# Performance work log

Hardware: AMD Instinct MI355X
Metric: run time of the kernel (lower is better)

The kernel has to match this reference:

```python
import jax, jax.numpy as jnp
import numpy as np

B, S, E, H = 2, 2048, 1024, 16
DH = E // H
SCALE = 1.0 / float(np.sqrt(E))  # note: original scales by 1/sqrt(hidden_dim), not head_dim


def _icl_mask(s):
    # triu(diagonal=0) is masked (-inf): only strictly-past positions visible,
    # except (0,0) which is explicitly unmasked so row 0 attends to itself.
    m = jnp.triu(jnp.ones((s, s), dtype=bool), k=0)
    return m.at[0, 0].set(False)


def setup_inputs() -> dict:
    key = jax.random.key(0)
    ks = jax.random.split(key, 7)
    mk = lambda k, shp: jax.random.normal(k, shp, dtype=jnp.float32)
    return {
        "q": mk(ks[0], (B, S, E)),
        "k": mk(ks[1], (B, S, E)),
        "v": mk(ks[2], (B, S, E)),
        "Wq": mk(ks[3], (E, E)) * 0.02,
        "Wk": mk(ks[4], (E, E)) * 0.02,
        "Wv": mk(ks[5], (E, E)) * 0.02,
        "Wo": mk(ks[6], (E, E)) * 0.02,
    }


def reference(q, k, v, Wq, Wk, Wv, Wo):
    b, s, e = q.shape
    h, dh = H, e // H
    # projections (nn.Linear: x @ W.T), split heads -> [b, h, s, dh]
    qh = (q @ Wq.T).reshape(b, s, h, dh).transpose(0, 2, 1, 3)
    kh = (k @ Wk.T).reshape(b, s, h, dh).transpose(0, 2, 1, 3)
    vh = (v @ Wv.T).reshape(b, s, h, dh).transpose(0, 2, 1, 3)
    scores = jnp.einsum("bhsd,bhtd->bhst", qh, kh) * SCALE  # [b,h,s,s]
    scores = jnp.where(_icl_mask(s), -jnp.inf, scores)
    probs = jax.nn.softmax(scores, axis=-1)
    out = jnp.einsum("bhst,bhtd->bhsd", probs, vh)
    out = out.transpose(0, 2, 1, 3).reshape(b, s, e)
    return out @ Wo.T
```

## Files before the change

kernel.cpp:

```cpp
#include <hip/hip_runtime.h>
#include <hip/hip_bf16.h>

typedef unsigned short u16;
typedef unsigned int u32;
typedef __bf16 bf16x8 __attribute__((ext_vector_type(8)));
typedef float float4_ __attribute__((ext_vector_type(4)));

#define B_ 2
#define S_ 2048
#define E_ 1024
#define H_ 16
#define DH_ 64
#define M_ (B_*S_)
#define SCALE_ 0.03125f
#define LOG2E_ 1.4426950408889634f

__device__ __forceinline__ u16 f2bf(float f) {
    unsigned int x = __float_as_uint(f);
    x += 0x7fffu + ((x >> 16) & 1u);
    return (u16)(x >> 16);
}

template <typename T> struct raw8;
template <> struct raw8<float> { float4_ lo, hi; };
template <> struct raw8<u16>   { bf16x8 v; };

__device__ __forceinline__ raw8<float> ldr8(const float* p) {
    raw8<float> r; const float4_* q = (const float4_*)p; r.lo = q[0]; r.hi = q[1]; return r;
}
__device__ __forceinline__ raw8<u16> ldr8(const u16* p) {
    raw8<u16> r; r.v = *(const bf16x8*)p; return r;
}
__device__ __forceinline__ bf16x8 cvt8(const raw8<u16>& r) { return r.v; }
__device__ __forceinline__ bf16x8 cvt8(const raw8<float>& r) {
    union { bf16x8 v; __hip_bfloat162 h[4]; } u;
    u.h[0] = __float22bfloat162_rn(float2{r.lo[0], r.lo[1]});
    u.h[1] = __float22bfloat162_rn(float2{r.lo[2], r.lo[3]});
    u.h[2] = __float22bfloat162_rn(float2{r.hi[0], r.hi[1]});
    u.h[3] = __float22bfloat162_rn(float2{r.hi[2], r.hi[3]});
    return u.v;
}
__device__ __forceinline__ bf16x8 ld8(const u16* p) { return *(const bf16x8*)p; }

__device__ __forceinline__ void async16(u16* lds, const u16* g) {
    __builtin_amdgcn_global_load_lds(
        (const __attribute__((address_space(1))) u32*)g,
        (__attribute__((address_space(3))) u32*)lds, 16, 0, 0);
}

__device__ __forceinline__ int swz32(int row, int col) {
    return row * 32 + ((((col >> 3) ^ (row & 3)) << 3) | (col & 7));
}

__global__ __launch_bounds__(256)
void convw_kernel(const float* __restrict__ Wq, const float* __restrict__ Wk,
                  const float* __restrict__ Wv, const float* __restrict__ Wo,
                  u16* __restrict__ Wqb, u16* __restrict__ Wkb,
                  u16* __restrict__ Wvb, u16* __restrict__ Wob) {
    const int which = blockIdx.y;
    const float* src = which == 0 ? Wq : which == 1 ? Wk : which == 2 ? Wv : Wo;
    u16* dst        = which == 0 ? Wqb : which == 1 ? Wkb : which == 2 ? Wvb : Wob;
    size_t off = ((size_t)blockIdx.x * 256 + threadIdx.x) * 8;
    *(bf16x8*)&dst[off] = cvt8(ldr8(&src[off]));
}

__global__ __launch_bounds__(256)
void proj_kernel(const float* __restrict__ q, const float* __restrict__ k, const float* __restrict__ v,
                 const u16* __restrict__ Wqb, const u16* __restrict__ Wkb, const u16* __restrict__ Wvb,
                 u16* __restrict__ Qh, u16* __restrict__ Kh, u16* __restrict__ Vt) {
    const int z = blockIdx.z;
    const float* A = (z == 0) ? q : (z == 1) ? k : v;
    const u16* Wb  = (z == 0) ? Wqb : (z == 1) ? Wkb : Wvb;
    u16* C         = (z == 0) ? Qh : (z == 1) ? Kh : Vt;
    const float cscale = (z == 0) ? SCALE_ : 1.0f;
    const int transV = (z == 2);
    const int bm = blockIdx.x * 128, bn = blockIdx.y * 128;

    __shared__ u16 As[2][128 * 32];
    __shared__ u16 Bs[2][128 * 32];

    const int tid  = threadIdx.x;
    const int lane = tid & 63;
    const int w    = tid >> 6;
    const int wr   = (w >> 1) * 64, wc = (w & 1) * 64;
    const int m16  = lane & 15, quad = lane >> 4, q4 = quad * 4;
    const int row0 = tid >> 2, kc0 = (tid & 3) * 8, row1 = row0 + 64;
    const int c1   = tid + 256;
    const int r1   = c1 >> 2;

    const u16* wg0 = &Wb[(size_t)(bn + row0) * 1024 + (size_t)(((tid & 3) ^ (row0 & 3)) * 8)];
    const u16* wg1 = &Wb[(size_t)(bn + r1)   * 1024 + (size_t)(((c1 & 3) ^ (r1 & 3)) * 8)];

    float4_ acc[4][4];
#pragma unroll
    for (int i = 0; i < 4; i++)
#pragma unroll
        for (int j = 0; j < 4; j++) acc[i][j] = (float4_){0.f, 0.f, 0.f, 0.f};

    raw8<float> pa0 = ldr8(&A[(size_t)(bm + row0) * 1024 + kc0]);
    raw8<float> pa1 = ldr8(&A[(size_t)(bm + row1) * 1024 + kc0]);

    async16((u16*)((char*)Bs[0] + (size_t)tid * 16), wg0);
    async16((u16*)((char*)Bs[0] + (size_t)c1 * 16), wg1);
    *(bf16x8*)&As[0][swz32(row0, kc0)] = cvt8(pa0);
    *(bf16x8*)&As[0][swz32(row1, kc0)] = cvt8(pa1);
    pa0 = ldr8(&A[(size_t)(bm + row0) * 1024 + 32 + kc0]);
    pa1 = ldr8(&A[(size_t)(bm + row1) * 1024 + 32 + kc0]);
    __syncthreads();

    auto step = [&](int t, const u16* Asc, const u16* Bsc, u16* Asn, u16* Bsn) {
        if (t < 31) {
            async16((u16*)((char*)Bsn + (size_t)tid * 16), wg0 + (t + 1) * 32);
            async16((u16*)((char*)Bsn + (size_t)c1 * 16), wg1 + (t + 1) * 32);
            *(bf16x8*)&Asn[swz32(row0, kc0)] = cvt8(pa0);
            *(bf16x8*)&Asn[swz32(row1, kc0)] = cvt8(pa1);
            if (t < 30) {
                pa0 = ldr8(&A[(size_t)(bm + row0) * 1024 + (t + 2) * 32 + kc0]);
                pa1 = ldr8(&A[(size_t)(bm + row1) * 1024 + (t + 2) * 32 + kc0]);
            }
        }
        __builtin_amdgcn_sched_barrier(0);
        bf16x8 af[4], bfr[4];
#pragma unroll
        for (int rt = 0; rt < 4; rt++)
            af[rt] = *(const bf16x8*)&Asc[swz32(wr + rt * 16 + m16, quad * 8)];
#pragma unroll
        for (int ct = 0; ct < 4; ct++)
            bfr[ct] = *(const bf16x8*)&Bsc[swz32(wc + ct * 16 + m16, quad * 8)];
#pragma unroll
        for (int rt = 0; rt < 4; rt++)
#pragma unroll
            for (int ct = 0; ct < 4; ct++)
                acc[rt][ct] = __builtin_amdgcn_mfma_f32_16x16x32_bf16(af[rt], bfr[ct], acc[rt][ct], 0, 0, 0);
        if (t < 31) __syncthreads();
    };

    for (int t = 0; t < 32; t += 2) {
        step(t,     As[0], Bs[0], As[1], Bs[1]);
        step(t + 1, As[1], Bs[1], As[0], Bs[0]);
    }

#pragma unroll
    for (int rt = 0; rt < 4; rt++)
#pragma unroll
        for (int ct = 0; ct < 4; ct++)
#pragma unroll
            for (int r = 0; r < 4; r++) {
                int row = bm + wr + rt * 16 + q4 + r;
                int col = bn + wc + ct * 16 + m16;
                u16 val = f2bf(acc[rt][ct][r] * cscale);
                if (!transV) {
                    C[(size_t)row * 1024 + col] = val;
                } else {
                    int bb = row >> 11, s = row & 2047;
                    C[((size_t)(bb * 1024 + col)) * 2048 + s] = val;
                }
            }
}

__global__ __launch_bounds__(256)
void out_kernel(const u16* __restrict__ AO, const u16* __restrict__ Wob, float* __restrict__ C) {
    const int bm = blockIdx.x * 128, bn = blockIdx.y * 64;

    __shared__ u16 As[2][128 * 32];
    __shared__ u16 Bs[2][64 * 32];

    const int tid  = threadIdx.x;
    const int lane = tid & 63;
    const int w    = tid >> 6;
    const int m16  = lane & 15, quad = lane >> 4, q4 = quad * 4;
    const int c1   = tid + 256;

    const int swc = (((tid & 3) ^ ((tid >> 2) & 3)) * 8);
    const u16* ag0 = &AO[(size_t)(bm + (tid >> 2)) * 1024 + swc];
    const u16* ag1 = &AO[(size_t)(bm + (c1 >> 2)) * 1024 + swc];
    const u16* bg  = &Wob[(size_t)(bn + (tid >> 2)) * 1024 + swc];

    float4_ acc[2][4];
#pragma unroll
    for (int i = 0; i < 2; i++)
#pragma unroll
        for (int j = 0; j < 4; j++) acc[i][j] = (float4_){0.f, 0.f, 0.f, 0.f};

    async16((u16*)((char*)As[0] + (size_t)tid * 16), ag0);
    async16((u16*)((char*)As[0] + (size_t)c1 * 16), ag1);
    async16((u16*)((char*)Bs[0] + (size_t)tid * 16), bg);
    __syncthreads();

    auto step = [&](int t, const u16* Asc, const u16* Bsc, u16* Asn, u16* Bsn) {
        if (t < 31) {
            async16((u16*)((char*)Asn + (size_t)tid * 16), ag0 + (t + 1) * 32);
            async16((u16*)((char*)Asn + (size_t)c1 * 16), ag1 + (t + 1) * 32);
            async16((u16*)((char*)Bsn + (size_t)tid * 16), bg + (t + 1) * 32);
        }
        __builtin_amdgcn_sched_barrier(0);
        bf16x8 af[2], bfr[4];
#pragma unroll
        for (int rt = 0; rt < 2; rt++)
            af[rt] = *(const bf16x8*)&Asc[swz32(w * 32 + rt * 16 + m16, quad * 8)];
#pragma unroll
        for (int ct = 0; ct < 4; ct++)
            bfr[ct] = *(const bf16x8*)&Bsc[swz32(ct * 16 + m16, quad * 8)];
#pragma unroll
        for (int rt = 0; rt < 2; rt++)
#pragma unroll
            for (int ct = 0; ct < 4; ct++)
                acc[rt][ct] = __builtin_amdgcn_mfma_f32_16x16x32_bf16(af[rt], bfr[ct], acc[rt][ct], 0, 0, 0);
        if (t < 31) __syncthreads();
    };

    for (int t = 0; t < 32; t += 2) {
        step(t,     As[0], Bs[0], As[1], Bs[1]);
        step(t + 1, As[1], Bs[1], As[0], Bs[0]);
    }

#pragma unroll
    for (int rt = 0; rt < 2; rt++)
#pragma unroll
        for (int ct = 0; ct < 4; ct++)
#pragma unroll
            for (int r = 0; r < 4; r++) {
                int row = bm + w * 32 + rt * 16 + q4 + r;
                int col = bn + ct * 16 + m16;
                C[(size_t)row * 1024 + col] = acc[rt][ct][r];
            }
}

__device__ __forceinline__ int sw64(int row, int col) {
    return row * 64 + ((((col >> 3) ^ (row & 7)) << 3) | (col & 7));
}

__global__ __launch_bounds__(256)
void attn_kernel(const u16* __restrict__ Qh, const u16* __restrict__ Kh,
                 const u16* __restrict__ Vt, u16* __restrict__ O) {
    const int h    = blockIdx.x;
    const int pair = blockIdx.y;
    const int tqA  = pair;
    const int tqB  = 31 - pair;
    const int b    = blockIdx.z;
    const int tid  = threadIdx.x;
    const int lane = tid & 63;
    const int w    = tid >> 6;
    const int m16  = lane & 15;
    const int quad = lane >> 4;
    const int q4   = quad * 4;

    __shared__ u16 Ks[2][64 * 64];
    __shared__ u16 Vs[2][64 * 64];
    __shared__ u16 PsA[64 * 64];
    __shared__ u16 PsB[64 * 64];

    const int srow0 = tid >> 3;
    const int skc0  = (tid & 7) * 8;
    const int sblk0 = ((skc0 >> 3) ^ (srow0 & 7)) << 3;
    const int srow1 = srow0 + 32;
    const int sblk1 = ((skc0 >> 3) ^ (srow1 & 7)) << 3;

    const size_t kbase = ((size_t)(b * S_)) * E_ + h * DH_;
    const size_t vbase = ((size_t)(b * 1024 + h * DH_)) * 2048;

    bf16x8 qfA[2], qfB[2];
    {
        const u16* qa = Qh + ((size_t)(b * S_ + tqA * 64 + w * 16 + m16)) * E_ + h * DH_;
        const u16* qb = Qh + ((size_t)(b * S_ + tqB * 64 + w * 16 + m16)) * E_ + h * DH_;
        qfA[0] = ld8(qa + quad * 8);  qfA[1] = ld8(qa + 32 + quad * 8);
        qfB[0] = ld8(qb + quad * 8);  qfB[1] = ld8(qb + 32 + quad * 8);
    }

    float lA[4] = {0.f, 0.f, 0.f, 0.f}, lB[4] = {0.f, 0.f, 0.f, 0.f};
    float4_ oA[4], oB[4];
#pragma unroll
    for (int dt = 0; dt < 4; dt++) { oA[dt] = (float4_){0.f,0.f,0.f,0.f}; oB[dt] = (float4_){0.f,0.f,0.f,0.f}; }

    *(bf16x8*)&Ks[0][srow0 * 64 + sblk0] = ld8(&Kh[kbase + (size_t)srow0 * E_ + skc0]);
    *(bf16x8*)&Ks[0][srow1 * 64 + sblk1] = ld8(&Kh[kbase + (size_t)srow1 * E_ + skc0]);
    *(bf16x8*)&Vs[0][srow0 * 64 + sblk0] = ld8(&Vt[vbase + (size_t)srow0 * 2048 + skc0]);
    *(bf16x8*)&Vs[0][srow1 * 64 + sblk1] = ld8(&Vt[vbase + (size_t)srow1 * 2048 + skc0]);
    __syncthreads();

    for (int t = 0; t <= tqB; t++) {
        const int cur = t & 1;

        bf16x8 kr0, kr1, vr0, vr1;
        const bool havepf = (t < tqB);
        if (havepf) {
            const size_t ko = kbase + (size_t)((t + 1) * 64) * E_;
            kr0 = ld8(&Kh[ko + (size_t)srow0 * E_ + skc0]);
            kr1 = ld8(&Kh[ko + (size_t)srow1 * E_ + skc0]);
            vr0 = ld8(&Vt[vbase + (size_t)srow0 * 2048 + (t + 1) * 64 + skc0]);
            vr1 = ld8(&Vt[vbase + (size_t)srow1 * 2048 + (t + 1) * 64 + skc0]);
        }

        auto process = [&](const bf16x8* qf, float* l_part, float4_* o_acc,
                           u16* Ps, int tqX) {
            const u16* Kc = &Ks[cur][0];
            const u16* Vc = &Vs[cur][0];
            float4_ sc[4];
#pragma unroll
            for (int ct = 0; ct < 4; ct++) sc[ct] = (float4_){0.f,0.f,0.f,0.f};
#pragma unroll
            for (int ks = 0; ks < 2; ks++)
#pragma unroll
                for (int ct = 0; ct < 4; ct++) {
                    bf16x8 kf = *(const bf16x8*)&Kc[sw64(ct * 16 + m16, ks * 32 + quad * 8)];
                    sc[ct] = __builtin_amdgcn_mfma_f32_16x16x32_bf16(qf[ks], kf, sc[ct], 0, 0, 0);
                }

            float p[4][4];
            if (t != tqX) {
#pragma unroll
                for (int ct = 0; ct < 4; ct++)
#pragma unroll
                    for (int r = 0; r < 4; r++) {
                        float pp = exp2f(sc[ct][r] * LOG2E_);
                        p[ct][r] = pp;
                        l_part[r] += pp;
                    }
            } else {
#pragma unroll
                for (int ct = 0; ct < 4; ct++)
#pragma unroll
                    for (int r = 0; r < 4; r++) {
                        int i_loc = w * 16 + q4 + r;
                        int j_loc = ct * 16 + m16;
                        bool allow = (j_loc < i_loc) || (tqX == 0 && i_loc == 0 && j_loc == 0);
                        float pp = allow ? exp2f(sc[ct][r] * LOG2E_) : 0.f;
                        p[ct][r] = pp;
                        l_part[r] += pp;
                    }
            }

#pragma unroll
            for (int ct = 0; ct < 4; ct++)
#pragma unroll
                for (int r = 0; r < 4; r++)
                    Ps[sw64(w * 16 + q4 + r, ct * 16 + m16)] = f2bf(p[ct][r]);

#pragma unroll
            for (int ks = 0; ks < 2; ks++) {
                bf16x8 pf = *(const bf16x8*)&Ps[sw64(w * 16 + m16, ks * 32 + quad * 8)];
#pragma unroll
                for (int dt = 0; dt < 4; dt++) {
                    bf16x8 vf = *(const bf16x8*)&Vc[sw64(dt * 16 + m16, ks * 32 + quad * 8)];
                    o_acc[dt] = __builtin_amdgcn_mfma_f32_16x16x32_bf16(pf, vf, o_acc[dt], 0, 0, 0);
                }
            }
        };

        process(qfB, lB, oB, PsB, tqB);
        if (t <= tqA) process(qfA, lA, oA, PsA, tqA);

        if (havepf) {
            const int nxt = cur ^ 1;
            *(bf16x8*)&Ks[nxt][srow0 * 64 + sblk0] = kr0;
            *(bf16x8*)&Ks[nxt][srow1 * 64 + sblk1] = kr1;
            *(bf16x8*)&Vs[nxt][srow0 * 64 + sblk0] = vr0;
            *(bf16x8*)&Vs[nxt][srow1 * 64 + sblk1] = vr1;
        }
        __syncthreads();
    }

    auto wrout = [&](const float4_* o_acc, const float* l_part, int tqX) {
        const size_t obase = ((size_t)(b * S_ + tqX * 64)) * E_ + h * DH_;
#pragma unroll
        for (int r = 0; r < 4; r++) {
            float l = l_part[r];
#pragma unroll
            for (int msk = 1; msk <= 8; msk <<= 1) l += __shfl_xor(l, msk);
            float inv_l = 1.0f / l;
            int row = w * 16 + q4 + r;
#pragma unroll
            for (int dt = 0; dt < 4; dt++) {
                int col = dt * 16 + m16;
                O[obase + (size_t)row * E_ + col] = f2bf(o_acc[dt][r] * inv_l);
            }
        }
    };
    wrout(oA, lA, tqA);
    wrout(oB, lB, tqB);
}

extern "C" void kernel_launch(void* const* d_in, const int* in_sizes, int n_in,
                              void* d_out, int out_size, void* d_ws, size_t ws_size,
                              hipStream_t stream) {
    const float* q  = (const float*)d_in[0];
    const float* k  = (const float*)d_in[1];
    const float* v  = (const float*)d_in[2];
    const float* Wq = (const float*)d_in[3];
    const float* Wk = (const float*)d_in[4];
    const float* Wv = (const float*)d_in[5];
    const float* Wo = (const float*)d_in[6];

    u16* ws  = (u16*)d_ws;
    u16* Qh  = ws;
    u16* Kh  = ws + (size_t)M_ * E_;
    u16* Vt  = ws + 2 * (size_t)M_ * E_;
    u16* AO  = ws + 3 * (size_t)M_ * E_;
    u16* Wqb = AO;
    u16* Wkb = AO + (size_t)E_ * E_;
    u16* Wvb = AO + 2 * (size_t)E_ * E_;
    u16* Wob = ws + 4 * (size_t)M_ * E_;

    dim3 blk(256);
    convw_kernel<<<dim3(512, 4), blk, 0, stream>>>(Wq, Wk, Wv, Wo, Wqb, Wkb, Wvb, Wob);
    proj_kernel<<<dim3(32, 8, 3), blk, 0, stream>>>(q, k, v, Wqb, Wkb, Wvb, Qh, Kh, Vt);
    attn_kernel<<<dim3(16, 16, 2), blk, 0, stream>>>(Qh, Kh, Vt, AO);
    out_kernel<<<dim3(32, 16), blk, 0, stream>>>(AO, Wob, (float*)d_out);
}
```

Baseline: 226.4 us.

## Pre-convert activations to bf16 and split attention query tiles across 512-thread blocks

Adds a separate conversion kernel that turns the q/k/v activations into bf16 so the projection GEMM can load both operands with async global-to-LDS copies instead of loading fp32 into registers and converting in the main loop. Xq and Xk are staged in the output buffer and Xv in spare workspace. The attention kernel now runs 512 threads per block, with each 4-wave half handling one of the paired query tiles at the same time, where before one set of waves processed both tiles in sequence. This costs an extra kernel launch and a full extra read and write pass over the activations. Waves on the shorter tile sit idle during later iterations but still hit the barriers.

```diff
diff --git a/kernel.cpp b/kernel.cpp
--- a/kernel.cpp
+++ b/kernel.cpp
@@ -12,6 +12,7 @@
 #define H_ 16
 #define DH_ 64
 #define M_ (B_*S_)
+#define E2_ (E_*E_)
 #define SCALE_ 0.03125f
 #define LOG2E_ 1.4426950408889634f
 
@@ -65,11 +66,22 @@
 }
 
 __global__ __launch_bounds__(256)
-void proj_kernel(const float* __restrict__ q, const float* __restrict__ k, const float* __restrict__ v,
+void convx_kernel(const float* __restrict__ q, const float* __restrict__ k,
+                  const float* __restrict__ v,
+                  u16* __restrict__ Xq, u16* __restrict__ Xk, u16* __restrict__ Xv) {
+    const int which = blockIdx.y;
+    const float* src = which == 0 ? q : which == 1 ? k : v;
+    u16* dst        = which == 0 ? Xq : which == 1 ? Xk : Xv;
+    size_t off = ((size_t)blockIdx.x * 256 + threadIdx.x) * 8;
+    *(bf16x8*)&dst[off] = cvt8(ldr8(&src[off]));
+}
+
+__global__ __launch_bounds__(256)
+void proj_kernel(const u16* __restrict__ Xq, const u16* __restrict__ Xk, const u16* __restrict__ Xv,
                  const u16* __restrict__ Wqb, const u16* __restrict__ Wkb, const u16* __restrict__ Wvb,
                  u16* __restrict__ Qh, u16* __restrict__ Kh, u16* __restrict__ Vt) {
     const int z = blockIdx.z;
-    const float* A = (z == 0) ? q : (z == 1) ? k : v;
+    const u16* A   = (z == 0) ? Xq : (z == 1) ? Xk : Xv;
     const u16* Wb  = (z == 0) ? Wqb : (z == 1) ? Wkb : Wvb;
     u16* C         = (z == 0) ? Qh : (z == 1) ? Kh : Vt;
     const float cscale = (z == 0) ? SCALE_ : 1.0f;
@@ -84,12 +96,13 @@
     const int w    = tid >> 6;
     const int wr   = (w >> 1) * 64, wc = (w & 1) * 64;
     const int m16  = lane & 15, quad = lane >> 4, q4 = quad * 4;
-    const int row0 = tid >> 2, kc0 = (tid & 3) * 8, row1 = row0 + 64;
-    const int c1   = tid + 256;
-    const int r1   = c1 >> 2;
-
-    const u16* wg0 = &Wb[(size_t)(bn + row0) * 1024 + (size_t)(((tid & 3) ^ (row0 & 3)) * 8)];
-    const u16* wg1 = &Wb[(size_t)(bn + r1)   * 1024 + (size_t)(((c1 & 3) ^ (r1 & 3)) * 8)];
+
+    const int row0 = tid >> 2, ch = tid & 3, row1 = row0 + 64;
+    const int csw  = ((ch ^ (row0 & 3)) * 8);
+    const u16* ag0 = &A[(size_t)(bm + row0) * 1024 + csw];
+    const u16* ag1 = &A[(size_t)(bm + row1) * 1024 + csw];
+    const u16* wg0 = &Wb[(size_t)(bn + row0) * 1024 + csw];
+    const u16* wg1 = &Wb[(size_t)(bn + row1) * 1024 + csw];
 
     float4_ acc[4][4];
 #pragma unroll
@@ -97,27 +110,19 @@
 #pragma unroll
         for (int j = 0; j < 4; j++) acc[i][j] = (float4_){0.f, 0.f, 0.f, 0.f};
 
-    raw8<float> pa0 = ldr8(&A[(size_t)(bm + row0) * 1024 + kc0]);
-    raw8<float> pa1 = ldr8(&A[(size_t)(bm + row1) * 1024 + kc0]);
-
+    async16((u16*)((char*)As[0] + (size_t)tid * 16), ag0);
+    async16((u16*)((char*)As[0] + (size_t)tid * 16 + 4096), ag1);
     async16((u16*)((char*)Bs[0] + (size_t)tid * 16), wg0);
-    async16((u16*)((char*)Bs[0] + (size_t)c1 * 16), wg1);
-    *(bf16x8*)&As[0][swz32(row0, kc0)] = cvt8(pa0);
-    *(bf16x8*)&As[0][swz32(row1, kc0)] = cvt8(pa1);
-    pa0 = ldr8(&A[(size_t)(bm + row0) * 1024 + 32 + kc0]);
-    pa1 = ldr8(&A[(size_t)(bm + row1) * 1024 + 32 + kc0]);
+    async16((u16*)((char*)Bs[0] + (size_t)tid * 16 + 4096), wg1);
     __syncthreads();
 
     auto step = [&](int t, const u16* Asc, const u16* Bsc, u16* Asn, u16* Bsn) {
         if (t < 31) {
-            async16((u16*)((char*)Bsn + (size_t)tid * 16), wg0 + (t + 1) * 32);
-            async16((u16*)((char*)Bsn + (size_t)c1 * 16), wg1 + (t + 1) * 32);
-            *(bf16x8*)&Asn[swz32(row0, kc0)] = cvt8(pa0);
-            *(bf16x8*)&Asn[swz32(row1, kc0)] = cvt8(pa1);
-            if (t < 30) {
-                pa0 = ldr8(&A[(size_t)(bm + row0) * 1024 + (t + 2) * 32 + kc0]);
-                pa1 = ldr8(&A[(size_t)(bm + row1) * 1024 + (t + 2) * 32 + kc0]);
-            }
+            const size_t ko = (size_t)(t + 1) * 32;
+            async16((u16*)((char*)Asn + (size_t)tid * 16), ag0 + ko);
+            async16((u16*)((char*)Asn + (size_t)tid * 16 + 4096), ag1 + ko);
+            async16((u16*)((char*)Bsn + (size_t)tid * 16), wg0 + ko);
+            async16((u16*)((char*)Bsn + (size_t)tid * 16 + 4096), wg1 + ko);
         }
         __builtin_amdgcn_sched_barrier(0);
         bf16x8 af[4], bfr[4];
@@ -230,74 +235,69 @@
     return row * 64 + ((((col >> 3) ^ (row & 7)) << 3) | (col & 7));
 }
 
-__global__ __launch_bounds__(256)
+__global__ __launch_bounds__(512)
 void attn_kernel(const u16* __restrict__ Qh, const u16* __restrict__ Kh,
                  const u16* __restrict__ Vt, u16* __restrict__ O) {
     const int h    = blockIdx.x;
     const int pair = blockIdx.y;
+    const int b    = blockIdx.z;
     const int tqA  = pair;
     const int tqB  = 31 - pair;
-    const int b    = blockIdx.z;
     const int tid  = threadIdx.x;
     const int lane = tid & 63;
     const int w    = tid >> 6;
+    const int half = w >> 2;
+    const int w4   = w & 3;
+    const int myTq = half ? tqB : tqA;
     const int m16  = lane & 15;
     const int quad = lane >> 4;
     const int q4   = quad * 4;
 
     __shared__ u16 Ks[2][64 * 64];
     __shared__ u16 Vs[2][64 * 64];
-    __shared__ u16 PsA[64 * 64];
-    __shared__ u16 PsB[64 * 64];
-
-    const int srow0 = tid >> 3;
-    const int skc0  = (tid & 7) * 8;
-    const int sblk0 = ((skc0 >> 3) ^ (srow0 & 7)) << 3;
-    const int srow1 = srow0 + 32;
-    const int sblk1 = ((skc0 >> 3) ^ (srow1 & 7)) << 3;
+    __shared__ u16 Ps[2][64 * 64];
+
+    const int srow = tid >> 3;
+    const int skc  = (tid & 7) * 8;
+    const int sblk = ((skc >> 3) ^ (srow & 7)) << 3;
 
     const size_t kbase = ((size_t)(b * S_)) * E_ + h * DH_;
     const size_t vbase = ((size_t)(b * 1024 + h * DH_)) * 2048;
 
-    bf16x8 qfA[2], qfB[2];
+    bf16x8 qf[2];
     {
-        const u16* qa = Qh + ((size_t)(b * S_ + tqA * 64 + w * 16 + m16)) * E_ + h * DH_;
-        const u16* qb = Qh + ((size_t)(b * S_ + tqB * 64 + w * 16 + m16)) * E_ + h * DH_;
-        qfA[0] = ld8(qa + quad * 8);  qfA[1] = ld8(qa + 32 + quad * 8);
-        qfB[0] = ld8(qb + quad * 8);  qfB[1] = ld8(qb + 32 + quad * 8);
+        const u16* qa = Qh + ((size_t)(b * S_ + myTq * 64 + w4 * 16 + m16)) * E_ + h * DH_;
+        qf[0] = ld8(qa + quad * 8);
+        qf[1] = ld8(qa + 32 + quad * 8);
     }
 
-    float lA[4] = {0.f, 0.f, 0.f, 0.f}, lB[4] = {0.f, 0.f, 0.f, 0.f};
-    float4_ oA[4], oB[4];
-#pragma unroll
-    for (int dt = 0; dt < 4; dt++) { oA[dt] = (float4_){0.f,0.f,0.f,0.f}; oB[dt] = (float4_){0.f,0.f,0.f,0.f}; }
-
-    *(bf16x8*)&Ks[0][srow0 * 64 + sblk0] = ld8(&Kh[kbase + (size_t)srow0 * E_ + skc0]);
-    *(bf16x8*)&Ks[0][srow1 * 64 + sblk1] = ld8(&Kh[kbase + (size_t)srow1 * E_ + skc0]);
-    *(bf16x8*)&Vs[0][srow0 * 64 + sblk0] = ld8(&Vt[vbase + (size_t)srow0 * 2048 + skc0]);
-    *(bf16x8*)&Vs[0][srow1 * 64 + sblk1] = ld8(&Vt[vbase + (size_t)srow1 * 2048 + skc0]);
+    float l_part[4] = {0.f, 0.f, 0.f, 0.f};
+    float4_ o_acc[4];
+#pragma unroll
+    for (int dt = 0; dt < 4; dt++) o_acc[dt] = (float4_){0.f, 0.f, 0.f, 0.f};
+
+    *(bf16x8*)&Ks[0][srow * 64 + sblk] = ld8(&Kh[kbase + (size_t)srow * E_ + skc]);
+    *(bf16x8*)&Vs[0][srow * 64 + sblk] = ld8(&Vt[vbase + (size_t)srow * 2048 + skc]);
     __syncthreads();
 
     for (int t = 0; t <= tqB; t++) {
         const int cur = t & 1;
 
-        bf16x8 kr0, kr1, vr0, vr1;
+        bf16x8 kr, vr;
         const bool havepf = (t < tqB);
         if (havepf) {
-            const size_t ko = kbase + (size_t)((t + 1) * 64) * E_;
-            kr0 = ld8(&Kh[ko + (size_t)srow0 * E_ + skc0]);
-            kr1 = ld8(&Kh[ko + (size_t)srow1 * E_ + skc0]);
-            vr0 = ld8(&Vt[vbase + (size_t)srow0 * 2048 + (t + 1) * 64 + skc0]);
-            vr1 = ld8(&Vt[vbase + (size_t)srow1 * 2048 + (t + 1) * 64 + skc0]);
-        }
-
-        auto process = [&](const bf16x8* qf, float* l_part, float4_* o_acc,
-                           u16* Ps, int tqX) {
+            kr = ld8(&Kh[kbase + (size_t)((t + 1) * 64 + srow) * E_ + skc]);
+            vr = ld8(&Vt[vbase + (size_t)srow * 2048 + (t + 1) * 64 + skc]);
+        }
+
+        if (t <= myTq) {
             const u16* Kc = &Ks[cur][0];
             const u16* Vc = &Vs[cur][0];
+            u16* Pm = &Ps[half][0];
+
             float4_ sc[4];
 #pragma unroll
-            for (int ct = 0; ct < 4; ct++) sc[ct] = (float4_){0.f,0.f,0.f,0.f};
+            for (int ct = 0; ct < 4; ct++) sc[ct] = (float4_){0.f, 0.f, 0.f, 0.f};
 #pragma unroll
             for (int ks = 0; ks < 2; ks++)
 #pragma unroll
@@ -307,7 +307,7 @@
                 }
 
             float p[4][4];
-            if (t != tqX) {
+            if (t != myTq) {
 #pragma unroll
                 for (int ct = 0; ct < 4; ct++)
 #pragma unroll
@@ -321,9 +321,9 @@
                 for (int ct = 0; ct < 4; ct++)
 #pragma unroll
                     for (int r = 0; r < 4; r++) {
-                        int i_loc = w * 16 + q4 + r;
+                        int i_loc = w4 * 16 + q4 + r;
                         int j_loc = ct * 16 + m16;
-                        bool allow = (j_loc < i_loc) || (tqX == 0 && i_loc == 0 && j_loc == 0);
+                        bool allow = (j_loc < i_loc) || (myTq == 0 && i_loc == 0 && j_loc == 0);
                         float pp = allow ? exp2f(sc[ct][r] * LOG2E_) : 0.f;
                         p[ct][r] = pp;
                         l_part[r] += pp;
@@ -334,50 +334,41 @@
             for (int ct = 0; ct < 4; ct++)
 #pragma unroll
                 for (int r = 0; r < 4; r++)
-                    Ps[sw64(w * 16 + q4 + r, ct * 16 + m16)] = f2bf(p[ct][r]);
+                    Pm[sw64(w4 * 16 + q4 + r, ct * 16 + m16)] = f2bf(p[ct][r]);
 
 #pragma unroll
             for (int ks = 0; ks < 2; ks++) {
-                bf16x8 pf = *(const bf16x8*)&Ps[sw64(w * 16 + m16, ks * 32 + quad * 8)];
+                bf16x8 pf = *(const bf16x8*)&Pm[sw64(w4 * 16 + m16, ks * 32 + quad * 8)];
 #pragma unroll
                 for (int dt = 0; dt < 4; dt++) {
                     bf16x8 vf = *(const bf16x8*)&Vc[sw64(dt * 16 + m16, ks * 32 + quad * 8)];
                     o_acc[dt] = __builtin_amdgcn_mfma_f32_16x16x32_bf16(pf, vf, o_acc[dt], 0, 0, 0);
                 }
             }
-        };
-
-        process(qfB, lB, oB, PsB, tqB);
-        if (t <= tqA) process(qfA, lA, oA, PsA, tqA);
+        }
 
         if (havepf) {
             const int nxt = cur ^ 1;
-            *(bf16x8*)&Ks[nxt][srow0 * 64 + sblk0] = kr0;
-            *(bf16x8*)&Ks[nxt][srow1 * 64 + sblk1] = kr1;
-            *(bf16x8*)&Vs[nxt][srow0 * 64 + sblk0] = vr0;
-            *(bf16x8*)&Vs[nxt][srow1 * 64 + sblk1] = vr1;
+            *(bf16x8*)&Ks[nxt][srow * 64 + sblk] = kr;
+            *(bf16x8*)&Vs[nxt][srow * 64 + sblk] = vr;
         }
         __syncthreads();
     }
 
-    auto wrout = [&](const float4_* o_acc, const float* l_part, int tqX) {
-        const size_t obase = ((size_t)(b * S_ + tqX * 64)) * E_ + h * DH_;
-#pragma unroll
-        for (int r = 0; r < 4; r++) {
-            float l = l_part[r];
-#pragma unroll
-            for (int msk = 1; msk <= 8; msk <<= 1) l += __shfl_xor(l, msk);
-            float inv_l = 1.0f / l;
-            int row = w * 16 + q4 + r;
-#pragma unroll
-            for (int dt = 0; dt < 4; dt++) {
-                int col = dt * 16 + m16;
-                O[obase + (size_t)row * E_ + col] = f2bf(o_acc[dt][r] * inv_l);
-            }
-        }
-    };
-    wrout(oA, lA, tqA);
-    wrout(oB, lB, tqB);
+    const size_t obase = ((size_t)(b * S_ + myTq * 64)) * E_ + h * DH_;
+#pragma unroll
+    for (int r = 0; r < 4; r++) {
+        float l = l_part[r];
+#pragma unroll
+        for (int msk = 1; msk <= 8; msk <<= 1) l += __shfl_xor(l, msk);
+        float inv_l = 1.0f / l;
+        int row = w4 * 16 + q4 + r;
+#pragma unroll
+        for (int dt = 0; dt < 4; dt++) {
+            int col = dt * 16 + m16;
+            O[obase + (size_t)row * E_ + col] = f2bf(o_acc[dt][r] * inv_l);
+        }
+    }
 }
 
 extern "C" void kernel_launch(void* const* d_in, const int* in_sizes, int n_in,
@@ -391,19 +382,24 @@
     const float* Wv = (const float*)d_in[5];
     const float* Wo = (const float*)d_in[6];
 
+    const size_t ME = (size_t)M_ * E_;
     u16* ws  = (u16*)d_ws;
     u16* Qh  = ws;
-    u16* Kh  = ws + (size_t)M_ * E_;
-    u16* Vt  = ws + 2 * (size_t)M_ * E_;
-    u16* AO  = ws + 3 * (size_t)M_ * E_;
+    u16* Kh  = ws + ME;
+    u16* Vt  = ws + 2 * ME;
+    u16* AO  = ws + 3 * ME;
     u16* Wqb = AO;
-    u16* Wkb = AO + (size_t)E_ * E_;
-    u16* Wvb = AO + 2 * (size_t)E_ * E_;
-    u16* Wob = ws + 4 * (size_t)M_ * E_;
+    u16* Wkb = AO + E2_;
+    u16* Wvb = AO + 2 * (size_t)E2_;
+    u16* Wob = ws + 4 * ME;
+    u16* Xv  = ws + 4 * ME + E2_;
+    u16* Xq  = (u16*)d_out;
+    u16* Xk  = Xq + ME;
 
     dim3 blk(256);
     convw_kernel<<<dim3(512, 4), blk, 0, stream>>>(Wq, Wk, Wv, Wo, Wqb, Wkb, Wvb, Wob);
-    proj_kernel<<<dim3(32, 8, 3), blk, 0, stream>>>(q, k, v, Wqb, Wkb, Wvb, Qh, Kh, Vt);
-    attn_kernel<<<dim3(16, 16, 2), blk, 0, stream>>>(Qh, Kh, Vt, AO);
+    convx_kernel<<<dim3(2048, 3), blk, 0, stream>>>(q, k, v, Xq, Xk, Xv);
+    proj_kernel<<<dim3(32, 8, 3), blk, 0, stream>>>(Xq, Xk, Xv, Wqb, Wkb, Wvb, Qh, Kh, Vt);
+    attn_kernel<<<dim3(16, 16, 2), dim3(512), 0, stream>>>(Qh, Kh, Vt, AO);
     out_kernel<<<dim3(32, 16), blk, 0, stream>>>(AO, Wob, (float*)d_out);
 }
```

After: 216.2 us. 4.5% less time.
